# Kernel optimization log

Hardware: AMD Instinct MI355X
Metric: run time of the kernel (lower is better)

Reference implementation:

```python
import jax, jax.numpy as jnp
import numpy as np

B, S, D_MODEL, H = 4, 4096, 1024, 16
HD = D_MODEL // H  # head_dim = 64


def setup_inputs() -> dict:
    key = jax.random.key(0)
    kq, kk, kv, kw, kb = jax.random.split(key, 5)
    Q = jax.random.normal(kq, (B, S, D_MODEL), dtype=jnp.float32)
    K = jax.random.normal(kk, (B, S, D_MODEL), dtype=jnp.float32)
    V = jax.random.normal(kv, (B, S, D_MODEL), dtype=jnp.float32)
    # out_proj: nn.Linear(d_model, d_model)
    lim = 1.0 / np.sqrt(D_MODEL)
    W_out = jax.random.uniform(kw, (D_MODEL, D_MODEL), jnp.float32, -lim, lim)
    b_out = jax.random.uniform(kb, (D_MODEL,), jnp.float32, -lim, lim)
    return {"Q": Q, "K": K, "V": V, "W_out": W_out, "b_out": b_out}


def reference(Q, K, V, W_out, b_out):
    b, s, d = Q.shape
    # split heads: [B, H, S, HD]
    Qh = Q.reshape(b, s, H, HD).transpose(0, 2, 1, 3)
    Kh = K.reshape(b, s, H, HD).transpose(0, 2, 1, 3)
    Vh = V.reshape(b, s, H, HD).transpose(0, 2, 1, 3)
    # linear attention reorder: KV = K^T V -> [B, H, HD, HD]
    KV = jnp.einsum('bhsd,bhse->bhde', Kh, Vh)
    # z = Q @ KV -> [B, H, S, HD]
    z = jnp.einsum('bhsd,bhde->bhse', Qh, KV)
    # merge heads -> [B, S, D]
    z = z.transpose(0, 2, 1, 3).reshape(b, s, d)
    # out_proj (torch Linear: x @ W^T + b, here W_out stored [out,in])
    return z @ W_out.T + b_out
```

## Files before the change

### kernel.cpp

```cpp
#include <hip/hip_runtime.h>
#include <hip/hip_bf16.h>

#define B_ 4
#define S_ 4096
#define DM 1024
#define H_ 16
#define HD 64
#define BH (B_*H_)
#define SPLIT 16
#define CHUNK (S_/SPLIT)

typedef __attribute__((ext_vector_type(8))) __bf16 bf16x8;
typedef __attribute__((ext_vector_type(4))) __bf16 bf16x4;
typedef __attribute__((ext_vector_type(4))) float f32x4;

#define MFMA16(a,b,c) __builtin_amdgcn_mfma_f32_16x16x32_bf16((a),(b),(c),0,0,0)

__device__ __forceinline__ void gload_lds16(const void* g, void* l) {
  __builtin_amdgcn_global_load_lds(
      (const __attribute__((address_space(1))) void*)g,
      (__attribute__((address_space(3))) void*)l, 16, 0, 0);
}

__global__ __launch_bounds__(256)
void k0_convw(const float* __restrict__ Wg, __bf16* __restrict__ Wb) {
  const size_t i = (size_t)blockIdx.x * 256 + threadIdx.x;
  f32x4 w = *reinterpret_cast<const f32x4*>(Wg + i * 4);
  bf16x4 o;
#pragma unroll
  for (int j = 0; j < 4; ++j) o[j] = (__bf16)w[j];
  *reinterpret_cast<bf16x4*>(Wb + i * 4) = o;
}

__global__ __launch_bounds__(256)
void k1_kv_partial(const float* __restrict__ Kg,
                   const float* __restrict__ Vg,
                   float* __restrict__ partial) {
  constexpr int LDP = 264;
  __shared__ __align__(16) __bf16 Kt[64 * LDP];
  __shared__ __align__(16) __bf16 Vt[64 * LDP];
  const int bid = blockIdx.x;
  const int split = bid >> 6;
  const int bh = bid & (BH - 1);
  const int b = bh >> 4, h = bh & 15;
  const int s0 = split * CHUNK;
  const int t = threadIdx.x;
  const float* Kbase = Kg + ((size_t)b * S_ + s0) * DM + h * HD;
  const float* Vbase = Vg + ((size_t)b * S_ + s0) * DM + h * HD;
  const int c = t & 15, sr = t >> 4;
  const int d0 = c * 4;
#pragma unroll
  for (int it = 0; it < 16; ++it) {
    const int s = it * 16 + sr;
    f32x4 kv = *reinterpret_cast<const f32x4*>(Kbase + (size_t)s * DM + d0);
    f32x4 vv = *reinterpret_cast<const f32x4*>(Vbase + (size_t)s * DM + d0);
#pragma unroll
    for (int j = 0; j < 4; ++j) {
      Kt[(d0 + j) * LDP + s] = (__bf16)kv[j];
      Vt[(d0 + j) * LDP + s] = (__bf16)vv[j];
    }
  }
  __syncthreads();
  const int w = t >> 6, l = t & 63, lr = l & 15, lg = l >> 4;
  f32x4 acc[4] = {};
#pragma unroll
  for (int ks = 0; ks < 8; ++ks) {
    bf16x8 a = *reinterpret_cast<const bf16x8*>(&Kt[(w * 16 + lr) * LDP + ks * 32 + lg * 8]);
#pragma unroll
    for (int n = 0; n < 4; ++n) {
      bf16x8 bb = *reinterpret_cast<const bf16x8*>(&Vt[(n * 16 + lr) * LDP + ks * 32 + lg * 8]);
      acc[n] = MFMA16(a, bb, acc[n]);
    }
  }
  float* dst = partial + ((size_t)(split * BH + bh) << 12);
#pragma unroll
  for (int n = 0; n < 4; ++n)
#pragma unroll
    for (int r = 0; r < 4; ++r) {
      const int d = w * 16 + lg * 4 + r;
      const int e = n * 16 + lr;
      dst[d * 64 + e] = acc[n][r];
    }
}

__global__ __launch_bounds__(256)
void k2_kv_reduce(const float* __restrict__ partial,
                  __bf16* __restrict__ kvt) {
  __shared__ float lds[64 * 65];
  const int bh = blockIdx.x, t = threadIdx.x;
#pragma unroll
  for (int i = 0; i < 16; ++i) {
    const int idx = i * 256 + t;
    float s = 0.f;
#pragma unroll
    for (int sp = 0; sp < SPLIT; ++sp)
      s += partial[((size_t)(sp * BH + bh) << 12) + idx];
    lds[(idx >> 6) * 65 + (idx & 63)] = s;
  }
  __syncthreads();
#pragma unroll
  for (int i = 0; i < 16; ++i) {
    const int idx = i * 256 + t;
    const int e = idx >> 6, d = idx & 63;
    kvt[((size_t)bh << 12) + idx] = (__bf16)lds[d * 65 + e];
  }
}

__global__ __launch_bounds__(256)
void k3_z(const float* __restrict__ Qg,
          const __bf16* __restrict__ kvt,
          __bf16* __restrict__ z) {
  const int bid = blockIdx.x;
  const int b = bid >> 6, sc = bid & 63;
  const int s0 = sc * 64;
  const int t = threadIdx.x, w = t >> 6, l = t & 63, lr = l & 15, lg = l >> 4;
  const float* qrow = Qg + ((size_t)b * S_ + s0 + w * 16 + lr) * DM;
#pragma unroll 1
  for (int h = 0; h < H_; ++h) {
    const __bf16* kvh = kvt + ((size_t)(b * H_ + h) << 12);
    f32x4 q0 = *reinterpret_cast<const f32x4*>(qrow + h * 64 + lg * 8);
    f32x4 q1 = *reinterpret_cast<const f32x4*>(qrow + h * 64 + lg * 8 + 4);
    f32x4 q2 = *reinterpret_cast<const f32x4*>(qrow + h * 64 + 32 + lg * 8);
    f32x4 q3 = *reinterpret_cast<const f32x4*>(qrow + h * 64 + 32 + lg * 8 + 4);
    bf16x8 a0, a1;
#pragma unroll
    for (int j = 0; j < 4; ++j) {
      a0[j] = (__bf16)q0[j]; a0[4 + j] = (__bf16)q1[j];
      a1[j] = (__bf16)q2[j]; a1[4 + j] = (__bf16)q3[j];
    }
    f32x4 acc[4] = {};
#pragma unroll
    for (int n = 0; n < 4; ++n) {
      bf16x8 b0 = *reinterpret_cast<const bf16x8*>(kvh + (n * 16 + lr) * 64 + lg * 8);
      bf16x8 b1 = *reinterpret_cast<const bf16x8*>(kvh + (n * 16 + lr) * 64 + 32 + lg * 8);
      acc[n] = MFMA16(a0, b0, acc[n]);
      acc[n] = MFMA16(a1, b1, acc[n]);
    }
#pragma unroll
    for (int n = 0; n < 4; ++n)
#pragma unroll
      for (int r = 0; r < 4; ++r) {
        const int srow = s0 + w * 16 + lg * 4 + r;
        z[((size_t)b * S_ + srow) * DM + h * 64 + n * 16 + lr] = (__bf16)acc[n][r];
      }
  }
}

__global__ __launch_bounds__(256)
void k4_out_gemm(const __bf16* __restrict__ zg,
                 const __bf16* __restrict__ Wb,
                 const float* __restrict__ biasg,
                 float* __restrict__ outg) {
  __shared__ __align__(16) __bf16 Alds[128 * 64];
  __shared__ __align__(16) __bf16 Blds[128 * 64];
  const int bid = blockIdx.x;
  const int mblk = bid & 127, nblk = bid >> 7;
  const int m0 = mblk * 128, n0 = nblk * 128;
  const int t = threadIdx.x, wid = t >> 6, l = t & 63, lr = l & 15, lg = l >> 4;
  const int wr = wid >> 1, wc = wid & 1;
  f32x4 acc[4][4] = {};

  for (int kt = 0; kt < 16; ++kt) {
    const int k0 = kt * 64;
#pragma unroll
    for (int it = 0; it < 4; ++it) {
      const int idx = it * 256 + t;
      const int row = idx >> 3, c = idx & 7;
      const int gc = c ^ (row & 7);
      const void* gA = (const void*)(zg + ((size_t)(m0 + row)) * DM + k0 + gc * 8);
      const void* gB = (const void*)(Wb + ((size_t)(n0 + row)) * DM + k0 + gc * 8);
      void* lA = (void*)((char*)Alds + (it * 256 + wid * 64) * 16);
      void* lB = (void*)((char*)Blds + (it * 256 + wid * 64) * 16);
      gload_lds16(gA, lA);
      gload_lds16(gB, lB);
    }
    __syncthreads();
#pragma unroll
    for (int ks = 0; ks < 2; ++ks) {
      bf16x8 af[4], bfr[4];
#pragma unroll
      for (int mt = 0; mt < 4; ++mt) {
        const int row = wr * 64 + mt * 16 + lr;
        const int ch = (ks * 4 + lg) ^ (row & 7);
        af[mt] = *reinterpret_cast<const bf16x8*>((const char*)Alds + row * 128 + ch * 16);
      }
#pragma unroll
      for (int nt = 0; nt < 4; ++nt) {
        const int row = wc * 64 + nt * 16 + lr;
        const int ch = (ks * 4 + lg) ^ (row & 7);
        bfr[nt] = *reinterpret_cast<const bf16x8*>((const char*)Blds + row * 128 + ch * 16);
      }
#pragma unroll
      for (int mt = 0; mt < 4; ++mt)
#pragma unroll
        for (int nt = 0; nt < 4; ++nt)
          acc[mt][nt] = MFMA16(af[mt], bfr[nt], acc[mt][nt]);
    }
    __syncthreads();
  }

#pragma unroll
  for (int nt = 0; nt < 4; ++nt) {
    const int colg = n0 + wc * 64 + nt * 16 + lr;
    const float bv = biasg[colg];
#pragma unroll
    for (int mt = 0; mt < 4; ++mt)
#pragma unroll
      for (int r = 0; r < 4; ++r) {
        const int rowg = m0 + wr * 64 + mt * 16 + lg * 4 + r;
        outg[(size_t)rowg * DM + colg] = acc[mt][nt][r] + bv;
      }
  }
}

extern "C" void kernel_launch(void* const* d_in, const int* in_sizes, int n_in,
                              void* d_out, int out_size, void* d_ws, size_t ws_size,
                              hipStream_t stream) {
  const float* Q = (const float*)d_in[0];
  const float* K = (const float*)d_in[1];
  const float* V = (const float*)d_in[2];
  const float* W = (const float*)d_in[3];
  const float* bias = (const float*)d_in[4];
  float* out = (float*)d_out;

  char* ws = (char*)d_ws;
  float* partial = (float*)ws;
  __bf16* kvt = (__bf16*)(ws + 16777216);
  __bf16* Wb  = (__bf16*)(ws + 16777216 + 524288);
  __bf16* z   = (__bf16*)(ws + 16777216 + 524288 + 2097152);

  hipLaunchKernelGGL(k0_convw, dim3(1024), dim3(256), 0, stream, W, Wb);
  hipLaunchKernelGGL(k1_kv_partial, dim3(SPLIT * BH), dim3(256), 0, stream, K, V, partial);
  hipLaunchKernelGGL(k2_kv_reduce, dim3(BH), dim3(256), 0, stream, partial, kvt);
  hipLaunchKernelGGL(k3_z, dim3(B_ * (S_ / 64)), dim3(256), 0, stream, Q, kvt, z);
  hipLaunchKernelGGL(k4_out_gemm, dim3(1024), dim3(256), 0, stream, z, Wb, bias, out);
}
```

Before: 128.8 us.

## Fold KV into output weights per batch and GEMM Q directly against them

Reassociates the computation as Q @ (blockdiag(KV) W^T), so a small new kernel builds a per-batch bf16 matrix U from KV and the fp32 W. The output GEMM then reads fp32 Q directly, converting it to bf16 in registers and prefetching the next tile. This removes the z intermediate write and read, the separate z kernel and the W conversion kernel. The reduce kernel is split across four times as many blocks and writes KV untransposed. The cost is extra per-batch GEMM work to build U, which is B times larger than W, and the output GEMM now loads twice the bytes for A because Q is fp32.

Result: slower. 134.3 us (+4.2%).

```diff
diff --git a/kernel.cpp b/kernel.cpp
--- a/kernel.cpp
+++ b/kernel.cpp
@@ -11,7 +11,6 @@
 #define CHUNK (S_/SPLIT)
 
 typedef __attribute__((ext_vector_type(8))) __bf16 bf16x8;
-typedef __attribute__((ext_vector_type(4))) __bf16 bf16x4;
 typedef __attribute__((ext_vector_type(4))) float f32x4;
 
 #define MFMA16(a,b,c) __builtin_amdgcn_mfma_f32_16x16x32_bf16((a),(b),(c),0,0,0)
@@ -20,16 +19,6 @@
   __builtin_amdgcn_global_load_lds(
       (const __attribute__((address_space(1))) void*)g,
       (__attribute__((address_space(3))) void*)l, 16, 0, 0);
-}
-
-__global__ __launch_bounds__(256)
-void k0_convw(const float* __restrict__ Wg, __bf16* __restrict__ Wb) {
-  const size_t i = (size_t)blockIdx.x * 256 + threadIdx.x;
-  f32x4 w = *reinterpret_cast<const f32x4*>(Wg + i * 4);
-  bf16x4 o;
-#pragma unroll
-  for (int j = 0; j < 4; ++j) o[j] = (__bf16)w[j];
-  *reinterpret_cast<bf16x4*>(Wb + i * 4) = o;
 }
 
 __global__ __launch_bounds__(256)
@@ -86,95 +75,120 @@
 __global__ __launch_bounds__(256)
 void k2_kv_reduce(const float* __restrict__ partial,
                   __bf16* __restrict__ kvt) {
-  __shared__ float lds[64 * 65];
-  const int bh = blockIdx.x, t = threadIdx.x;
-#pragma unroll
-  for (int i = 0; i < 16; ++i) {
-    const int idx = i * 256 + t;
+  const int bid = blockIdx.x;
+  const int bh = bid >> 2, q = bid & 3;
+  const int t = threadIdx.x;
+#pragma unroll
+  for (int i = 0; i < 4; ++i) {
+    const int idx = q * 1024 + i * 256 + t;
     float s = 0.f;
 #pragma unroll
     for (int sp = 0; sp < SPLIT; ++sp)
       s += partial[((size_t)(sp * BH + bh) << 12) + idx];
-    lds[(idx >> 6) * 65 + (idx & 63)] = s;
-  }
-  __syncthreads();
-#pragma unroll
-  for (int i = 0; i < 16; ++i) {
-    const int idx = i * 256 + t;
-    const int e = idx >> 6, d = idx & 63;
-    kvt[((size_t)bh << 12) + idx] = (__bf16)lds[d * 65 + e];
-  }
-}
-
-__global__ __launch_bounds__(256)
-void k3_z(const float* __restrict__ Qg,
-          const __bf16* __restrict__ kvt,
-          __bf16* __restrict__ z) {
-  const int bid = blockIdx.x;
-  const int b = bid >> 6, sc = bid & 63;
-  const int s0 = sc * 64;
+    kvt[((size_t)bh << 12) + idx] = (__bf16)s;
+  }
+}
+
+__global__ __launch_bounds__(256)
+void k25_u(const float* __restrict__ Wg,
+           const __bf16* __restrict__ kvt,
+           __bf16* __restrict__ Ut) {
+  const int bid = blockIdx.x;
+  const int bh = bid >> 2, nblk = bid & 3;
+  const int b = bh >> 4, h = bh & 15;
   const int t = threadIdx.x, w = t >> 6, l = t & 63, lr = l & 15, lg = l >> 4;
-  const float* qrow = Qg + ((size_t)b * S_ + s0 + w * 16 + lr) * DM;
-#pragma unroll 1
-  for (int h = 0; h < H_; ++h) {
-    const __bf16* kvh = kvt + ((size_t)(b * H_ + h) << 12);
-    f32x4 q0 = *reinterpret_cast<const f32x4*>(qrow + h * 64 + lg * 8);
-    f32x4 q1 = *reinterpret_cast<const f32x4*>(qrow + h * 64 + lg * 8 + 4);
-    f32x4 q2 = *reinterpret_cast<const f32x4*>(qrow + h * 64 + 32 + lg * 8);
-    f32x4 q3 = *reinterpret_cast<const f32x4*>(qrow + h * 64 + 32 + lg * 8 + 4);
-    bf16x8 a0, a1;
-#pragma unroll
-    for (int j = 0; j < 4; ++j) {
-      a0[j] = (__bf16)q0[j]; a0[4 + j] = (__bf16)q1[j];
-      a1[j] = (__bf16)q2[j]; a1[4 + j] = (__bf16)q3[j];
-    }
-    f32x4 acc[4] = {};
-#pragma unroll
-    for (int n = 0; n < 4; ++n) {
-      bf16x8 b0 = *reinterpret_cast<const bf16x8*>(kvh + (n * 16 + lr) * 64 + lg * 8);
-      bf16x8 b1 = *reinterpret_cast<const bf16x8*>(kvh + (n * 16 + lr) * 64 + 32 + lg * 8);
-      acc[n] = MFMA16(a0, b0, acc[n]);
-      acc[n] = MFMA16(a1, b1, acc[n]);
-    }
-#pragma unroll
-    for (int n = 0; n < 4; ++n)
+  const int n0w = nblk * 256 + w * 64;
+  const __bf16* kvb = kvt + ((size_t)bh << 12);
+  f32x4 acc[4][4] = {};
+#pragma unroll
+  for (int ks = 0; ks < 2; ++ks) {
+    bf16x8 bfr[4];
+#pragma unroll
+    for (int nf = 0; nf < 4; ++nf)
+      bfr[nf] = *reinterpret_cast<const bf16x8*>(kvb + (nf * 16 + lr) * 64 + ks * 32 + lg * 8);
+#pragma unroll
+    for (int mf = 0; mf < 4; ++mf) {
+      const int n = n0w + mf * 16 + lr;
+      const float* wp = Wg + (size_t)n * DM + h * 64 + ks * 32 + lg * 8;
+      f32x4 w0 = *reinterpret_cast<const f32x4*>(wp);
+      f32x4 w1 = *reinterpret_cast<const f32x4*>(wp + 4);
+      bf16x8 af;
+#pragma unroll
+      for (int j = 0; j < 4; ++j) { af[j] = (__bf16)w0[j]; af[4 + j] = (__bf16)w1[j]; }
+#pragma unroll
+      for (int nf = 0; nf < 4; ++nf)
+        acc[mf][nf] = MFMA16(af, bfr[nf], acc[mf][nf]);
+    }
+  }
+  __bf16* ub = Ut + ((size_t)b << 20);
+#pragma unroll
+  for (int mf = 0; mf < 4; ++mf)
+#pragma unroll
+    for (int nf = 0; nf < 4; ++nf)
 #pragma unroll
       for (int r = 0; r < 4; ++r) {
-        const int srow = s0 + w * 16 + lg * 4 + r;
-        z[((size_t)b * S_ + srow) * DM + h * 64 + n * 16 + lr] = (__bf16)acc[n][r];
-      }
-  }
-}
-
-__global__ __launch_bounds__(256)
-void k4_out_gemm(const __bf16* __restrict__ zg,
-                 const __bf16* __restrict__ Wb,
+        const int n = n0w + mf * 16 + lg * 4 + r;
+        ub[(size_t)n * DM + h * 64 + nf * 16 + lr] = (__bf16)acc[mf][nf][r];
+      }
+}
+
+__global__ __launch_bounds__(256)
+void k4_out_gemm(const float* __restrict__ Qg,
+                 const __bf16* __restrict__ Ut,
                  const float* __restrict__ biasg,
                  float* __restrict__ outg) {
   __shared__ __align__(16) __bf16 Alds[128 * 64];
   __shared__ __align__(16) __bf16 Blds[128 * 64];
   const int bid = blockIdx.x;
-  const int mblk = bid & 127, nblk = bid >> 7;
+  const int b = bid >> 8, rem = bid & 255;
+  const int nblk = rem >> 5, mblk = rem & 31;
   const int m0 = mblk * 128, n0 = nblk * 128;
   const int t = threadIdx.x, wid = t >> 6, l = t & 63, lr = l & 15, lg = l >> 4;
   const int wr = wid >> 1, wc = wid & 1;
+  const float* Qb = Qg + (size_t)b * S_ * DM;
+  const __bf16* Ub = Ut + ((size_t)b << 20);
   f32x4 acc[4][4] = {};
+
+  const int srow = (t >> 3), sc = t & 7;
+  bf16x8 aregs[4];
+
+#pragma unroll
+  for (int it = 0; it < 4; ++it) {
+    const int row = it * 32 + srow;
+    const float* qp = Qb + (size_t)(m0 + row) * DM + sc * 8;
+    f32x4 lo = *reinterpret_cast<const f32x4*>(qp);
+    f32x4 hi = *reinterpret_cast<const f32x4*>(qp + 4);
+#pragma unroll
+    for (int j = 0; j < 4; ++j) { aregs[it][j] = (__bf16)lo[j]; aregs[it][4 + j] = (__bf16)hi[j]; }
+  }
 
   for (int kt = 0; kt < 16; ++kt) {
     const int k0 = kt * 64;
 #pragma unroll
     for (int it = 0; it < 4; ++it) {
-      const int idx = it * 256 + t;
-      const int row = idx >> 3, c = idx & 7;
-      const int gc = c ^ (row & 7);
-      const void* gA = (const void*)(zg + ((size_t)(m0 + row)) * DM + k0 + gc * 8);
-      const void* gB = (const void*)(Wb + ((size_t)(n0 + row)) * DM + k0 + gc * 8);
-      void* lA = (void*)((char*)Alds + (it * 256 + wid * 64) * 16);
-      void* lB = (void*)((char*)Blds + (it * 256 + wid * 64) * 16);
-      gload_lds16(gA, lA);
-      gload_lds16(gB, lB);
+      const int row = it * 32 + srow;
+      const int gc = sc ^ (row & 7);
+      gload_lds16((const void*)(Ub + (size_t)(n0 + row) * DM + k0 + gc * 8),
+                  (void*)((char*)Blds + (it * 256 + wid * 64) * 16));
+    }
+#pragma unroll
+    for (int it = 0; it < 4; ++it) {
+      const int row = it * 32 + srow;
+      const int ch = sc ^ (row & 7);
+      *reinterpret_cast<bf16x8*>((char*)Alds + row * 128 + ch * 16) = aregs[it];
     }
     __syncthreads();
+    if (kt < 15) {
+#pragma unroll
+      for (int it = 0; it < 4; ++it) {
+        const int row = it * 32 + srow;
+        const float* qp = Qb + (size_t)(m0 + row) * DM + (k0 + 64) + sc * 8;
+        f32x4 lo = *reinterpret_cast<const f32x4*>(qp);
+        f32x4 hi = *reinterpret_cast<const f32x4*>(qp + 4);
+#pragma unroll
+        for (int j = 0; j < 4; ++j) { aregs[it][j] = (__bf16)lo[j]; aregs[it][4 + j] = (__bf16)hi[j]; }
+      }
+    }
 #pragma unroll
     for (int ks = 0; ks < 2; ++ks) {
       bf16x8 af[4], bfr[4];
@@ -208,7 +222,7 @@
 #pragma unroll
       for (int r = 0; r < 4; ++r) {
         const int rowg = m0 + wr * 64 + mt * 16 + lg * 4 + r;
-        outg[(size_t)rowg * DM + colg] = acc[mt][nt][r] + bv;
+        outg[((size_t)b * S_ + rowg) * DM + colg] = acc[mt][nt][r] + bv;
       }
   }
 }
@@ -226,12 +240,10 @@
   char* ws = (char*)d_ws;
   float* partial = (float*)ws;
   __bf16* kvt = (__bf16*)(ws + 16777216);
-  __bf16* Wb  = (__bf16*)(ws + 16777216 + 524288);
-  __bf16* z   = (__bf16*)(ws + 16777216 + 524288 + 2097152);
-
-  hipLaunchKernelGGL(k0_convw, dim3(1024), dim3(256), 0, stream, W, Wb);
+  __bf16* Ut  = (__bf16*)(ws + 16777216 + 524288);
+
   hipLaunchKernelGGL(k1_kv_partial, dim3(SPLIT * BH), dim3(256), 0, stream, K, V, partial);
-  hipLaunchKernelGGL(k2_kv_reduce, dim3(BH), dim3(256), 0, stream, partial, kvt);
-  hipLaunchKernelGGL(k3_z, dim3(B_ * (S_ / 64)), dim3(256), 0, stream, Q, kvt, z);
-  hipLaunchKernelGGL(k4_out_gemm, dim3(1024), dim3(256), 0, stream, z, Wb, bias, out);
-}
+  hipLaunchKernelGGL(k2_kv_reduce, dim3(BH * 4), dim3(256), 0, stream, partial, kvt);
+  hipLaunchKernelGGL(k25_u, dim3(BH * 4), dim3(256), 0, stream, W, kvt, Ut);
+  hipLaunchKernelGGL(k4_out_gemm, dim3(1024), dim3(256), 0, stream, Q, Ut, bias, out);
+}
```
